# Performance work log

Hardware: AMD Instinct MI355X
Metric: run time of the kernel (lower is better)

## Reference

```python
import jax, jax.numpy as jnp
import numpy as np

S, M, E = 8192, 2048, 64          # tokens, model_dim, num_experts
CAP = 2 * S // E                   # GShard top-2 capacity = 2S/E = 256


def setup_inputs() -> dict:
    key = jax.random.key(0)
    k1, k2, k3 = jax.random.split(key, 3)
    x = jax.random.normal(k1, (S, M), dtype=jnp.float32)
    # torch.nn.Linear weight layout: [out_features, in_features] = [E, M]
    wg = jax.random.normal(k2, (E, M), dtype=jnp.float32) * np.float32(1.0 / np.sqrt(M))
    u = jax.random.uniform(k3, (S, E), dtype=jnp.float32, minval=1e-6, maxval=1.0 - 1e-6)
    gumbel = -jnp.log(-jnp.log(u))  # standard Gumbel(0,1) noise for 2nd-expert sampling
    return {"x": x, "wg": wg, "gumbel": gumbel}


def top2gating(logits, gumbel):
    # logits: [S, E]
    gates = jax.nn.softmax(logits.astype(jnp.float32), axis=1)

    # top-1 expert
    idx1 = jnp.argmax(gates, axis=1)                        # [S]
    mask1 = jax.nn.one_hot(idx1, E, dtype=jnp.int32)        # [S, E]

    # top-2 expert: argmax over gumbel-noised logits with top-1 masked out
    logits_except1 = jnp.where(mask1.astype(bool), -jnp.inf, logits + gumbel)
    idx2 = jnp.argmax(logits_except1, axis=1)
    mask2 = jax.nn.one_hot(idx2, E, dtype=jnp.int32)

    # positions within each expert's buffer (capacity cumsum)
    loc1 = jnp.cumsum(mask1, axis=0) - 1                    # [S, E]
    loc2 = jnp.cumsum(mask2, axis=0) - 1 + jnp.sum(mask1, axis=0, keepdims=True)

    # load-balancing auxiliary loss
    me = jnp.mean(gates, axis=0)                            # [E]
    ce = jnp.mean(mask1.astype(jnp.float32), axis=0)        # [E]
    l_aux = jnp.mean(me * ce) * np.float32(E * E)

    # drop tokens that exceed capacity
    mask1 = mask1 * (loc1 < CAP).astype(jnp.int32)
    mask2 = mask2 * (loc2 < CAP).astype(jnp.int32)

    loc1_s = jnp.sum(loc1 * mask1, axis=1)                  # [S]
    loc2_s = jnp.sum(loc2 * mask2, axis=1)

    m1f = mask1.astype(jnp.float32)
    m2f = mask2.astype(jnp.float32)

    # normalized top-2 gate values
    g1 = jnp.sum(gates * m1f, axis=1)                       # [S]
    g2 = jnp.sum(gates * m2f, axis=1)
    denom = jnp.maximum(g1 + g2, jnp.finfo(jnp.float32).eps)
    g1 = g1 / denom
    g2 = g2 / denom

    gates1 = g1[:, None] * m1f                              # [S, E]
    gates2 = g2[:, None] * m2f

    loc1_sc = jax.nn.one_hot(loc1_s, CAP, dtype=jnp.float32)  # [S, C]
    loc2_sc = jax.nn.one_hot(loc2_s, CAP, dtype=jnp.float32)

    combine_weights = (jnp.einsum('se,sc->sec', gates1, loc1_sc)
                       + jnp.einsum('se,sc->sec', gates2, loc2_sc))  # [S, E, C]
    dispatch_mask = combine_weights > 0
    return l_aux, combine_weights, dispatch_mask


def reference(x, wg, gumbel):
    logits = x @ wg.T                                       # [S, E]
    return top2gating(logits, gumbel)
```

## Files before the change

### kernel.cpp

```cpp
#include <hip/hip_runtime.h>
#include <cstdint>
#include <cstddef>

#define S_TOK 8192
#define MDIM  2048
#define NEXP  64
#define CAPTY 256
#define NCHUNK 128

__global__ __launch_bounds__(256) void gemm_logits(
    const float* __restrict__ x, const float* __restrict__ wg,
    float* __restrict__ outA, float* __restrict__ outB) {
  __shared__ float xs[64][36];
  __shared__ float wsh[64][36];
  const int half = blockIdx.y;
  const int rowBase = blockIdx.x * 64;
  const int kHalf = half * 1024;
  const int t = threadIdx.x;
  const int tx = t & 15;
  const int ty = t >> 4;
  float acc[4][4] = {{0.f}};

  const int rStage = t >> 3;
  const int cStage = (t & 7) << 2;

  for (int kt = 0; kt < 1024; kt += 32) {
    const int kBase = kHalf + kt;
    for (int rr = rStage; rr < 64; rr += 32) {
      float4 xv = *reinterpret_cast<const float4*>(
          &x[(size_t)(rowBase + rr) * MDIM + kBase + cStage]);
      *reinterpret_cast<float4*>(&xs[rr][cStage]) = xv;
      float4 wv = *reinterpret_cast<const float4*>(
          &wg[(size_t)rr * MDIM + kBase + cStage]);
      *reinterpret_cast<float4*>(&wsh[rr][cStage]) = wv;
    }
    __syncthreads();
#pragma unroll
    for (int k = 0; k < 32; k += 4) {
      float4 xa[4], wb[4];
#pragma unroll
      for (int a = 0; a < 4; ++a)
        xa[a] = *reinterpret_cast<const float4*>(&xs[ty * 4 + a][k]);
#pragma unroll
      for (int b = 0; b < 4; ++b)
        wb[b] = *reinterpret_cast<const float4*>(&wsh[tx + 16 * b][k]);
#pragma unroll
      for (int a = 0; a < 4; ++a)
#pragma unroll
        for (int b = 0; b < 4; ++b) {
          acc[a][b] += xa[a].x * wb[b].x;
          acc[a][b] += xa[a].y * wb[b].y;
          acc[a][b] += xa[a].z * wb[b].z;
          acc[a][b] += xa[a].w * wb[b].w;
        }
    }
    __syncthreads();
  }
  float* out = half ? outB : outA;
#pragma unroll
  for (int a = 0; a < 4; ++a)
#pragma unroll
    for (int b = 0; b < 4; ++b)
      out[(size_t)(rowBase + ty * 4 + a) * NEXP + tx + 16 * b] = acc[a][b];
}

__global__ __launch_bounds__(1024) void gating(
    const float* __restrict__ la, const float* __restrict__ lb,
    const float* __restrict__ gum,
    int* __restrict__ e1o, int* __restrict__ e2o,
    float* __restrict__ g1o, float* __restrict__ g2o,
    float* __restrict__ me_sum) {
  __shared__ float me_l[NEXP];
  const int t = threadIdx.x;
  if (t < NEXP) me_l[t] = 0.f;
  __syncthreads();

  const int w = t >> 6;
  const int lane = t & 63;
  const int s = blockIdx.x * 16 + w;
  const size_t base = (size_t)s * NEXP + lane;

  const float l = la[base] + lb[base];
  const float gn = gum[base];

  float m = l;
#pragma unroll
  for (int d = 1; d < 64; d <<= 1) m = fmaxf(m, __shfl_xor(m, d, 64));
  const float p = expf(l - m);
  float sum = p;
#pragma unroll
  for (int d = 1; d < 64; d <<= 1) sum += __shfl_xor(sum, d, 64);

  unsigned long long b1 = __ballot(l == m);
  const int e1 = __ffsll(b1) - 1;

  const float y = (lane == e1) ? -INFINITY : (l + gn);
  float m2 = y;
#pragma unroll
  for (int d = 1; d < 64; d <<= 1) m2 = fmaxf(m2, __shfl_xor(m2, d, 64));
  unsigned long long b2 = __ballot(y == m2);
  const int e2 = __ffsll(b2) - 1;

  const float p1 = __shfl(p, e1, 64);
  const float p2 = __shfl(p, e2, 64);

  atomicAdd(&me_l[lane], p / sum);

  if (lane == 0) {
    e1o[s] = e1;
    e2o[s] = e2;
    g1o[s] = p1;
    g2o[s] = p2;
  }
  __syncthreads();
  if (t < NEXP) atomicAdd(&me_sum[t], me_l[t]);
}

__global__ __launch_bounds__(64) void rank_chunks(
    const int* __restrict__ e1, const int* __restrict__ e2,
    int* __restrict__ w1, int* __restrict__ w2,
    int* __restrict__ hist1, int* __restrict__ hist2) {
  const int c = blockIdx.x;
  const int lane = threadIdx.x;
  const int s = c * 64 + lane;
  const int a = e1[s];
  const int b = e2[s];
  const unsigned long long lt = (1ull << lane) - 1ull;
  int r1 = 0, r2 = 0;
  for (int e = 0; e < NEXP; ++e) {
    unsigned long long m1 = __ballot(a == e);
    unsigned long long m2 = __ballot(b == e);
    if (a == e) r1 = __popcll(m1 & lt);
    if (b == e) r2 = __popcll(m2 & lt);
    if (lane == e) {
      hist1[c * NEXP + e] = __popcll(m1);
      hist2[c * NEXP + e] = __popcll(m2);
    }
  }
  w1[s] = r1;
  w2[s] = r2;
}

__global__ __launch_bounds__(64) void prefix_aux(
    const int* __restrict__ hist1, const int* __restrict__ hist2,
    const float* __restrict__ me_sum,
    int* __restrict__ off1, int* __restrict__ off2,
    float* __restrict__ out0) {
  const int e = threadIdx.x;
  int run = 0;
  for (int c = 0; c < NCHUNK; ++c) {
    off1[c * NEXP + e] = run;
    run += hist1[c * NEXP + e];
  }
  const int tot1 = run;
  int run2 = tot1;
  for (int c = 0; c < NCHUNK; ++c) {
    off2[c * NEXP + e] = run2;
    run2 += hist2[c * NEXP + e];
  }
  float la = me_sum[e] * (float)tot1;
#pragma unroll
  for (int d = 1; d < 64; d <<= 1) la += __shfl_xor(la, d, 64);
  if (e == 0)
    out0[0] = la * (float)NEXP / ((float)S_TOK * (float)S_TOK);
}

__global__ __launch_bounds__(256) void scatter(
    const int* __restrict__ e1, const int* __restrict__ e2,
    const int* __restrict__ w1, const int* __restrict__ w2,
    const float* __restrict__ g1r, const float* __restrict__ g2r,
    const int* __restrict__ off1, const int* __restrict__ off2,
    float* __restrict__ out) {
  const int s = blockIdx.x * 256 + threadIdx.x;
  const int c = s >> 6;
  const int a = e1[s];
  const int b = e2[s];
  const int l1 = off1[c * NEXP + a] + w1[s];
  const int l2 = off2[c * NEXP + b] + w2[s];
  const bool k1 = l1 < CAPTY;
  const bool k2 = l2 < CAPTY;
  float p1 = k1 ? g1r[s] : 0.f;
  float p2 = k2 ? g2r[s] : 0.f;
  const float denom = p1 + p2;
  if (denom > 0.f) {
    const float inv = 1.f / denom;
    float* cw = out + 1;
    float* dm = out + 1 + (size_t)S_TOK * NEXP * CAPTY;
    const size_t rowb = (size_t)s * NEXP * CAPTY;
    if (k1) {
      const size_t i1 = rowb + (size_t)a * CAPTY + l1;
      cw[i1] = p1 * inv;
      dm[i1] = 1.f;
    }
    if (k2) {
      const size_t i2 = rowb + (size_t)b * CAPTY + l2;
      cw[i2] = p2 * inv;
      dm[i2] = 1.f;
    }
  }
}

extern "C" void kernel_launch(void* const* d_in, const int* in_sizes, int n_in,
                              void* d_out, int out_size, void* d_ws,
                              size_t ws_size, hipStream_t stream) {
  const float* x = (const float*)d_in[0];
  const float* wg = (const float*)d_in[1];
  const float* gum = (const float*)d_in[2];
  float* out = (float*)d_out;

  char* w = (char*)d_ws;
  size_t off = 0;
  float* logitsA = (float*)(w + off); off += (size_t)S_TOK * NEXP * 4;
  float* logitsB = (float*)(w + off); off += (size_t)S_TOK * NEXP * 4;
  int*   e1   = (int*)(w + off); off += (size_t)S_TOK * 4;
  int*   e2   = (int*)(w + off); off += (size_t)S_TOK * 4;
  float* g1r  = (float*)(w + off); off += (size_t)S_TOK * 4;
  float* g2r  = (float*)(w + off); off += (size_t)S_TOK * 4;
  int*   w1   = (int*)(w + off); off += (size_t)S_TOK * 4;
  int*   w2   = (int*)(w + off); off += (size_t)S_TOK * 4;
  int*   hist1 = (int*)(w + off); off += (size_t)NCHUNK * NEXP * 4;
  int*   hist2 = (int*)(w + off); off += (size_t)NCHUNK * NEXP * 4;
  int*   off1 = (int*)(w + off); off += (size_t)NCHUNK * NEXP * 4;
  int*   off2 = (int*)(w + off); off += (size_t)NCHUNK * NEXP * 4;
  float* me_sum = (float*)(w + off); off += NEXP * 4;

  hipMemsetAsync(d_out, 0, (size_t)out_size * sizeof(float), stream);
  hipMemsetAsync(me_sum, 0, NEXP * sizeof(float), stream);

  gemm_logits<<<dim3(S_TOK / 64, 2), 256, 0, stream>>>(x, wg, logitsA, logitsB);
  gating<<<S_TOK / 16, 1024, 0, stream>>>(logitsA, logitsB, gum, e1, e2, g1r,
                                          g2r, me_sum);
  rank_chunks<<<NCHUNK, 64, 0, stream>>>(e1, e2, w1, w2, hist1, hist2);
  prefix_aux<<<1, 64, 0, stream>>>(hist1, hist2, me_sum, off1, off2, out);
  scatter<<<S_TOK / 256, 256, 0, stream>>>(e1, e2, w1, w2, g1r, g2r, off1,
                                           off2, out);
}
```

Measured before the change: 1.163 ms.

## Fuse output zero-fill into GEMM launch and merge gating with chunk ranking

Replaces the hipMemsetAsync of the large output with extra blocks in the logits GEMM kernel that write zeros with float4 stores, so the fill can overlap the GEMM. The gating and per-chunk ranking kernels are merged into one kernel per 64-token chunk, with e1/e2 kept in shared memory. The global atomic accumulation of the softmax means is replaced by per-chunk partials that prefix_aux sums, which also removes the second memset. This saves launches and memset overhead, but the fill loop hardcodes the output size and its cost is still bound by memory bandwidth.

```diff
diff --git a/kernel.cpp b/kernel.cpp
--- a/kernel.cpp
+++ b/kernel.cpp
@@ -8,15 +8,35 @@
 #define CAPTY 256
 #define NCHUNK 128
 
-__global__ __launch_bounds__(256) void gemm_logits(
+#define GEMM_BLOCKS 256
+#define FILL_BLOCKS 2048
+
+__global__ __launch_bounds__(256) void fill_and_gemm(
     const float* __restrict__ x, const float* __restrict__ wg,
-    float* __restrict__ outA, float* __restrict__ outB) {
+    float* __restrict__ outA, float* __restrict__ outB,
+    float* __restrict__ out) {
+  const int bid = blockIdx.x;
+  const int t = threadIdx.x;
+
+  if (bid >= GEMM_BLOCKS) {
+    const int fb = bid - GEMM_BLOCKS;
+    float4 z = {0.f, 0.f, 0.f, 0.f};
+    float4* o4 = reinterpret_cast<float4*>(out);
+    size_t idx = (size_t)fb * 256 + t;
+#pragma unroll 8
+    for (int i = 0; i < 128; ++i) {
+      o4[idx] = z;
+      idx += (size_t)FILL_BLOCKS * 256;
+    }
+    if (fb == 0 && t == 0) out[268435456] = 0.f;
+    return;
+  }
+
   __shared__ float xs[64][36];
   __shared__ float wsh[64][36];
-  const int half = blockIdx.y;
-  const int rowBase = blockIdx.x * 64;
+  const int half = bid & 1;
+  const int rowBase = (bid >> 1) * 64;
   const int kHalf = half * 1024;
-  const int t = threadIdx.x;
   const int tx = t & 15;
   const int ty = t >> 4;
   float acc[4][4] = {{0.f}};
@@ -56,94 +76,98 @@
     }
     __syncthreads();
   }
-  float* out = half ? outB : outA;
+  float* o = half ? outB : outA;
 #pragma unroll
   for (int a = 0; a < 4; ++a)
 #pragma unroll
     for (int b = 0; b < 4; ++b)
-      out[(size_t)(rowBase + ty * 4 + a) * NEXP + tx + 16 * b] = acc[a][b];
-}
-
-__global__ __launch_bounds__(1024) void gating(
+      o[(size_t)(rowBase + ty * 4 + a) * NEXP + tx + 16 * b] = acc[a][b];
+}
+
+__global__ __launch_bounds__(1024) void gate_rank(
     const float* __restrict__ la, const float* __restrict__ lb,
     const float* __restrict__ gum,
     int* __restrict__ e1o, int* __restrict__ e2o,
     float* __restrict__ g1o, float* __restrict__ g2o,
-    float* __restrict__ me_sum) {
+    float* __restrict__ me_part,
+    int* __restrict__ w1, int* __restrict__ w2,
+    int* __restrict__ hist1, int* __restrict__ hist2) {
   __shared__ float me_l[NEXP];
+  __shared__ int e1_l[64], e2_l[64];
+  const int c = blockIdx.x;
   const int t = threadIdx.x;
+  const int w = t >> 6;
+  const int lane = t & 63;
   if (t < NEXP) me_l[t] = 0.f;
   __syncthreads();
 
-  const int w = t >> 6;
-  const int lane = t & 63;
-  const int s = blockIdx.x * 16 + w;
-  const size_t base = (size_t)s * NEXP + lane;
-
-  const float l = la[base] + lb[base];
-  const float gn = gum[base];
-
-  float m = l;
-#pragma unroll
-  for (int d = 1; d < 64; d <<= 1) m = fmaxf(m, __shfl_xor(m, d, 64));
-  const float p = expf(l - m);
-  float sum = p;
-#pragma unroll
-  for (int d = 1; d < 64; d <<= 1) sum += __shfl_xor(sum, d, 64);
-
-  unsigned long long b1 = __ballot(l == m);
-  const int e1 = __ffsll(b1) - 1;
-
-  const float y = (lane == e1) ? -INFINITY : (l + gn);
-  float m2 = y;
-#pragma unroll
-  for (int d = 1; d < 64; d <<= 1) m2 = fmaxf(m2, __shfl_xor(m2, d, 64));
-  unsigned long long b2 = __ballot(y == m2);
-  const int e2 = __ffsll(b2) - 1;
-
-  const float p1 = __shfl(p, e1, 64);
-  const float p2 = __shfl(p, e2, 64);
-
-  atomicAdd(&me_l[lane], p / sum);
-
-  if (lane == 0) {
-    e1o[s] = e1;
-    e2o[s] = e2;
-    g1o[s] = p1;
-    g2o[s] = p2;
-  }
+  float me_acc = 0.f;
+#pragma unroll
+  for (int i = 0; i < 4; ++i) {
+    const int s = c * 64 + w * 4 + i;
+    const size_t base = (size_t)s * NEXP + lane;
+    const float l = la[base] + lb[base];
+    const float gn = gum[base];
+
+    float m = l;
+#pragma unroll
+    for (int d = 1; d < 64; d <<= 1) m = fmaxf(m, __shfl_xor(m, d, 64));
+    const float p = expf(l - m);
+    float sum = p;
+#pragma unroll
+    for (int d = 1; d < 64; d <<= 1) sum += __shfl_xor(sum, d, 64);
+
+    unsigned long long b1 = __ballot(l == m);
+    const int e1 = __ffsll(b1) - 1;
+
+    const float y = (lane == e1) ? -INFINITY : (l + gn);
+    float m2 = y;
+#pragma unroll
+    for (int d = 1; d < 64; d <<= 1) m2 = fmaxf(m2, __shfl_xor(m2, d, 64));
+    unsigned long long b2 = __ballot(y == m2);
+    const int e2 = __ffsll(b2) - 1;
+
+    const float p1 = __shfl(p, e1, 64);
+    const float p2 = __shfl(p, e2, 64);
+
+    me_acc += p / sum;
+
+    if (lane == 0) {
+      e1o[s] = e1;
+      e2o[s] = e2;
+      g1o[s] = p1;
+      g2o[s] = p2;
+      e1_l[w * 4 + i] = e1;
+      e2_l[w * 4 + i] = e2;
+    }
+  }
+  atomicAdd(&me_l[lane], me_acc);
   __syncthreads();
-  if (t < NEXP) atomicAdd(&me_sum[t], me_l[t]);
-}
-
-__global__ __launch_bounds__(64) void rank_chunks(
-    const int* __restrict__ e1, const int* __restrict__ e2,
-    int* __restrict__ w1, int* __restrict__ w2,
-    int* __restrict__ hist1, int* __restrict__ hist2) {
-  const int c = blockIdx.x;
-  const int lane = threadIdx.x;
-  const int s = c * 64 + lane;
-  const int a = e1[s];
-  const int b = e2[s];
-  const unsigned long long lt = (1ull << lane) - 1ull;
-  int r1 = 0, r2 = 0;
-  for (int e = 0; e < NEXP; ++e) {
-    unsigned long long m1 = __ballot(a == e);
-    unsigned long long m2 = __ballot(b == e);
-    if (a == e) r1 = __popcll(m1 & lt);
-    if (b == e) r2 = __popcll(m2 & lt);
-    if (lane == e) {
-      hist1[c * NEXP + e] = __popcll(m1);
-      hist2[c * NEXP + e] = __popcll(m2);
-    }
-  }
-  w1[s] = r1;
-  w2[s] = r2;
+
+  if (w == 0) {
+    const int a = e1_l[lane];
+    const int b = e2_l[lane];
+    const unsigned long long lt = (1ull << lane) - 1ull;
+    int r1 = 0, r2 = 0;
+    for (int e = 0; e < NEXP; ++e) {
+      unsigned long long m1 = __ballot(a == e);
+      unsigned long long m2 = __ballot(b == e);
+      if (a == e) r1 = __popcll(m1 & lt);
+      if (b == e) r2 = __popcll(m2 & lt);
+      if (lane == e) {
+        hist1[c * NEXP + e] = __popcll(m1);
+        hist2[c * NEXP + e] = __popcll(m2);
+      }
+    }
+    w1[c * 64 + lane] = r1;
+    w2[c * 64 + lane] = r2;
+  }
+  if (t < NEXP) me_part[c * NEXP + t] = me_l[t];
 }
 
 __global__ __launch_bounds__(64) void prefix_aux(
     const int* __restrict__ hist1, const int* __restrict__ hist2,
-    const float* __restrict__ me_sum,
+    const float* __restrict__ me_part,
     int* __restrict__ off1, int* __restrict__ off2,
     float* __restrict__ out0) {
   const int e = threadIdx.x;
@@ -158,7 +182,9 @@
     off2[c * NEXP + e] = run2;
     run2 += hist2[c * NEXP + e];
   }
-  float la = me_sum[e] * (float)tot1;
+  float ms = 0.f;
+  for (int c = 0; c < NCHUNK; ++c) ms += me_part[c * NEXP + e];
+  float la = ms * (float)tot1;
 #pragma unroll
   for (int d = 1; d < 64; d <<= 1) la += __shfl_xor(la, d, 64);
   if (e == 0)
@@ -222,16 +248,13 @@
   int*   hist2 = (int*)(w + off); off += (size_t)NCHUNK * NEXP * 4;
   int*   off1 = (int*)(w + off); off += (size_t)NCHUNK * NEXP * 4;
   int*   off2 = (int*)(w + off); off += (size_t)NCHUNK * NEXP * 4;
-  float* me_sum = (float*)(w + off); off += NEXP * 4;
-
-  hipMemsetAsync(d_out, 0, (size_t)out_size * sizeof(float), stream);
-  hipMemsetAsync(me_sum, 0, NEXP * sizeof(float), stream);
-
-  gemm_logits<<<dim3(S_TOK / 64, 2), 256, 0, stream>>>(x, wg, logitsA, logitsB);
-  gating<<<S_TOK / 16, 1024, 0, stream>>>(logitsA, logitsB, gum, e1, e2, g1r,
-                                          g2r, me_sum);
-  rank_chunks<<<NCHUNK, 64, 0, stream>>>(e1, e2, w1, w2, hist1, hist2);
-  prefix_aux<<<1, 64, 0, stream>>>(hist1, hist2, me_sum, off1, off2, out);
+  float* me_part = (float*)(w + off); off += (size_t)NCHUNK * NEXP * 4;
+
+  fill_and_gemm<<<GEMM_BLOCKS + FILL_BLOCKS, 256, 0, stream>>>(
+      x, wg, logitsA, logitsB, out);
+  gate_rank<<<NCHUNK, 1024, 0, stream>>>(logitsA, logitsB, gum, e1, e2, g1r,
+                                         g2r, me_part, w1, w2, hist1, hist2);
+  prefix_aux<<<1, 64, 0, stream>>>(hist1, hist2, me_part, off1, off2, out);
   scatter<<<S_TOK / 256, 256, 0, stream>>>(e1, e2, w1, w2, g1r, g2r, off1,
                                            off2, out);
 }
```

Result: no change. 1.149 ms (-1.2%).
